# Kernel tuning notes

Measured on AMD Instinct MI355X. Metric: run time of the kernel, lower is better.

## Reference

```python
import jax, jax.numpy as jnp
import numpy as np
from jax import lax

EPS = 1e-5
DN = ('NCHW', 'OIHW', 'NCHW')


def setup_inputs() -> dict:
    key = jax.random.key(0)
    ks = jax.random.split(key, 16)
    B = 8192
    # uniform(0,1): every pixel nonzero => all voxels active => sparse conv == dense conv
    x = jax.random.uniform(ks[0], (B, 1, 28, 28), dtype=jnp.float32)

    def conv_params(kw, kb, c_in, c_out, k):
        scale = 1.0 / np.sqrt(c_in * k * k)
        w = jax.random.normal(kw, (c_out, c_in, k, k), dtype=jnp.float32) * scale
        b = jax.random.normal(kb, (c_out,), dtype=jnp.float32) * scale
        return w, b

    w0, b0 = conv_params(ks[1], ks[2], 1, 32, 3)
    w1, b1 = conv_params(ks[3], ks[4], 32, 64, 2)
    w2, b2 = conv_params(ks[5], ks[6], 64, 128, 2)
    # BatchNorm affine params (init: gamma=1, beta=0)
    g0, be0 = jnp.ones((32,), jnp.float32), jnp.zeros((32,), jnp.float32)
    g1, be1 = jnp.ones((64,), jnp.float32), jnp.zeros((64,), jnp.float32)
    g2, be2 = jnp.ones((128,), jnp.float32), jnp.zeros((128,), jnp.float32)
    w_fc = jax.random.normal(ks[7], (10, 128), dtype=jnp.float32) * (1.0 / np.sqrt(128))
    b_fc = jax.random.normal(ks[8], (10,), dtype=jnp.float32) * (1.0 / np.sqrt(128))
    return dict(x=x, w0=w0, b0=b0, g0=g0, be0=be0,
                w1=w1, b1=b1, g1=g1, be1=be1,
                w2=w2, b2=b2, g2=g2, be2=be2,
                w_fc=w_fc, b_fc=b_fc)


def _conv_bn_relu(x, w, b, g, be, stride, padding):
    # sparse conv on fully-active grid == dense conv
    y = lax.conv_general_dilated(x, w, (stride, stride), padding,
                                 dimension_numbers=DN)
    y = y + b[None, :, None, None]
    # BatchNorm1d over (N_active, C) == stats over batch+spatial (biased var)
    mean = jnp.mean(y, axis=(0, 2, 3))
    var = jnp.var(y, axis=(0, 2, 3))
    y = (y - mean[None, :, None, None]) * lax.rsqrt(var + EPS)[None, :, None, None]
    y = y * g[None, :, None, None] + be[None, :, None, None]
    return jax.nn.relu(y)


def reference(x, w0, b0, g0, be0, w1, b1, g1, be1, w2, b2, g2, be2, w_fc, b_fc):
    h = _conv_bn_relu(x, w0, b0, g0, be0, 1, 'SAME')    # (B,32,28,28)
    h = _conv_bn_relu(h, w1, b1, g1, be1, 2, 'VALID')   # (B,64,14,14)
    h = _conv_bn_relu(h, w2, b2, g2, be2, 2, 'VALID')   # (B,128,7,7)
    pooled = jnp.mean(h, axis=(2, 3))                    # AdaptiveAvgPool2d(1)+Flatten
    return pooled @ w_fc.T + b_fc                        # (B, n_classes)
```

## Files before the change

kernel.cpp:

```cpp
#include <hip/hip_runtime.h>
#include <hip/hip_bf16.h>

typedef __bf16 bf16x8 __attribute__((ext_vector_type(8)));
typedef float  f32x4  __attribute__((ext_vector_type(4)));
typedef float  f32x2  __attribute__((ext_vector_type(2)));

#define BSZ 8192

__device__ __constant__ int d_base2[9] = {0, 5, 9, 13, 16, 19, 21, 23, 24};

__global__ __launch_bounds__(256) void k_stats0(const float* __restrict__ x,
                                                float* __restrict__ part0,
                                                const float* __restrict__ w1,
                                                const float* __restrict__ w2,
                                                __bf16* __restrict__ w1b,
                                                __bf16* __restrict__ w2b) {
    __shared__ float sred[4 * 59];
    const int tid = threadIdx.x;
    {
        int t = blockIdx.x * 256 + tid;
        if (t < 8192) {
            int oc = t >> 7, k = t & 127, c = k & 31, d = k >> 5;
            w1b[t] = (__bf16)w1[oc * 128 + c * 4 + d];
        }
        if (t < 32768) {
            int oc = t >> 8, k = t & 255, c = k & 63, d = k >> 6;
            w2b[t] = (__bf16)w2[oc * 256 + c * 4 + d];
        }
    }
    const int base2[9] = {0, 5, 9, 13, 16, 19, 21, 23, 24};
    const int rsz[9]   = {5, 4, 4, 3, 3, 2, 2, 1, 1};
    f32x2 a2[25];
    float ax[9];
#pragma unroll
    for (int i = 0; i < 25; i++) a2[i] = (f32x2){0.f, 0.f};
#pragma unroll
    for (int i = 0; i < 9; i++) ax[i] = 0.f;
    const int total = BSZ * 784;
    for (int p = blockIdx.x * 256 + tid; p < total; p += gridDim.x * 256) {
        int b = p / 784, pix = p - b * 784;
        int y = pix / 28, xx = pix - y * 28;
        const float* xb = x + (long)b * 784;
        float nv[9];
#pragma unroll
        for (int dy = 0; dy < 3; dy++) {
            int yy = y + dy - 1;
#pragma unroll
            for (int dx = 0; dx < 3; dx++) {
                int x2 = xx + dx - 1;
                nv[dy * 3 + dx] = (yy >= 0 && yy < 28 && x2 >= 0 && x2 < 28) ? xb[yy * 28 + x2] : 0.f;
            }
        }
#pragma unroll
        for (int t = 0; t < 9; t++) {
            float vt = nv[t];
            ax[t] += vt;
            f32x2 vv = {vt, vt};
#pragma unroll
            for (int pp2 = 0; pp2 < 5; pp2++) {
                if (pp2 < rsz[t]) {
                    int u = t + 2 * pp2;
                    f32x2 nn = {nv[u], (u + 1 < 9) ? nv[u + 1] : 0.f};
                    a2[base2[t] + pp2] = __builtin_elementwise_fma(vv, nn, a2[base2[t] + pp2]);
                }
            }
        }
    }
    float outv[59];
#pragma unroll
    for (int i = 0; i < 50; i++) outv[i] = a2[i >> 1][i & 1];
#pragma unroll
    for (int i = 0; i < 9; i++) outv[50 + i] = ax[i];
#pragma unroll
    for (int i = 0; i < 59; i++) {
        float v = outv[i];
        v += __shfl_xor(v, 1);  v += __shfl_xor(v, 2);  v += __shfl_xor(v, 4);
        v += __shfl_xor(v, 8);  v += __shfl_xor(v, 16); v += __shfl_xor(v, 32);
        outv[i] = v;
    }
    const int l = tid & 63, w = tid >> 6;
    if (l == 0) {
#pragma unroll
        for (int i = 0; i < 59; i++) sred[w * 59 + i] = outv[i];
    }
    __syncthreads();
    if (tid < 59)
        part0[blockIdx.x * 64 + tid] = sred[tid] + sred[59 + tid] + sred[118 + tid] + sred[177 + tid];
}

__global__ void k_fin0(const float* __restrict__ part0, const float* __restrict__ w0,
                       const float* __restrict__ g0, const float* __restrict__ be0,
                       float* __restrict__ abc0) {
    __shared__ float red[4 * 59];
    int t = threadIdx.x, c = t & 63, g = t >> 6;
    if (c < 59) {
        float acc = 0.f;
        for (int i = g; i < 1024; i += 4) acc += part0[i * 64 + c];
        red[g * 59 + c] = acc;
    }
    __syncthreads();
    if (t < 59) red[t] = red[t] + red[59 + t] + red[118 + t] + red[177 + t];
    __syncthreads();
    if (t < 32) {
        const int base2[9] = {0, 5, 9, 13, 16, 19, 21, 23, 24};
        float wv[9];
#pragma unroll
        for (int tap = 0; tap < 9; tap++) wv[tap] = w0[t * 9 + tap];
        float sum = 0.f, sq = 0.f;
#pragma unroll
        for (int ta = 0; ta < 9; ta++) {
            sum = fmaf(wv[ta], red[50 + ta], sum);
#pragma unroll
            for (int u = ta; u < 9; u++) {
                float coef = (u == ta) ? 1.f : 2.f;
                float Mv = red[2 * base2[ta] + (u - ta)];
                sq = fmaf(coef * wv[ta] * wv[u], Mv, sq);
            }
        }
        float cnt = (float)BSZ * 784.f;
        float mean = sum / cnt;
        float var = sq / cnt - mean * mean;
        float A = g0[t] * rsqrtf(var + 1e-5f);
#pragma unroll
        for (int tap = 0; tap < 9; tap++)
            abc0[(t >> 3) * 72 + tap * 8 + (t & 7)] = A * wv[tap];
        abc0[288 + t] = be0[t] - mean * A;
    }
}

__global__ __launch_bounds__(256) void k_conv01(const float* __restrict__ x,
                                                const float* __restrict__ abc0,
                                                const __bf16* __restrict__ w1b,
                                                __bf16* __restrict__ h1,
                                                float* __restrict__ part1) {
    __shared__ float xs[30 * 30];
    __shared__ __attribute__((aligned(16))) __bf16 sAt[2][16 * 136];
    const int tid = threadIdx.x;
    if (tid < 116) {
        int idx;
        if (tid < 30)      idx = tid;
        else if (tid < 60) idx = 29 * 30 + (tid - 30);
        else if (tid < 88) idx = (tid - 60 + 1) * 30;
        else               idx = (tid - 88 + 1) * 30 + 29;
        xs[idx] = 0.f;
    }
    const int pgu = __builtin_amdgcn_readfirstlane(tid >> 6);
    const f32x2* wfp = (const f32x2*)(abc0 + pgu * 72);
    f32x2 wf2[36];
#pragma unroll
    for (int i = 0; i < 36; i++) wf2[i] = wfp[i];
    const f32x2* c2p = (const f32x2*)(abc0 + 288 + pgu * 8);
    f32x2 c2[4];
#pragma unroll
    for (int j = 0; j < 4; j++) c2[j] = c2p[j];

    const int pi = tid & 15, pd = (tid >> 4) & 3;
    const int w = tid >> 6, l = tid & 63, q = l >> 4, n = l & 15;
    const int oc = w * 16 + n;
    bf16x8 fbv[4];
#pragma unroll
    for (int kc = 0; kc < 4; kc++)
        fbv[kc] = *(const bf16x8*)&w1b[oc * 128 + kc * 32 + q * 8];
    const f32x2 zero2 = {0.f, 0.f};

    for (int img = 0; img < 4; img++) {
        const int b = blockIdx.x * 4 + img;
        const f32x4* xb4 = (const f32x4*)(x + (long)b * 784);
        if (tid < 196) {
            int yy = tid / 7, xx4 = (tid - yy * 7) * 4;
            f32x4 v4 = xb4[tid];
            float* dst = &xs[(yy + 1) * 30 + xx4 + 1];
            dst[0] = v4[0]; dst[1] = v4[1]; dst[2] = v4[2]; dst[3] = v4[3];
        }
        __syncthreads();
        f32x2 st_s = zero2, st_q = zero2;
        __bf16* hb = h1 + (long)b * 12544 + (q * 4) * 64 + oc;
        for (int mt = 0; mt < 13; mt++) {
            __bf16* dst = &sAt[mt & 1][pi * 136 + pd * 32 + pgu * 8];
            int m = mt * 16 + pi;
            bf16x8 pk;
            if (m < 196) {
                int my = m / 14, mx = m - my * 14;
                int y0 = my * 2 + (pd >> 1), x0 = mx * 2 + (pd & 1);
                float nv[9];
#pragma unroll
                for (int dy = 0; dy < 3; dy++)
#pragma unroll
                    for (int dx = 0; dx < 3; dx++)
                        nv[dy * 3 + dx] = xs[(y0 + dy) * 30 + x0 + dx];
                f32x2 a2[4];
#pragma unroll
                for (int j = 0; j < 4; j++) a2[j] = c2[j];
#pragma unroll
                for (int t = 0; t < 9; t++) {
                    f32x2 vv = {nv[t], nv[t]};
#pragma unroll
                    for (int j = 0; j < 4; j++)
                        a2[j] = __builtin_elementwise_fma(vv, wf2[t * 4 + j], a2[j]);
                }
#pragma unroll
                for (int j = 0; j < 4; j++) {
                    f32x2 mv = __builtin_elementwise_max(a2[j], zero2);
                    pk[2 * j]     = (__bf16)mv[0];
                    pk[2 * j + 1] = (__bf16)mv[1];
                }
            } else {
#pragma unroll
                for (int j = 0; j < 8; j++) pk[j] = (__bf16)0.0f;
            }
            *(bf16x8*)dst = pk;
            __syncthreads();
            const __bf16* sa = &sAt[mt & 1][n * 136 + q * 8];
            f32x4 acc = {0.f, 0.f, 0.f, 0.f};
#pragma unroll
            for (int kc = 0; kc < 4; kc++) {
                bf16x8 fav = *(const bf16x8*)&sa[kc * 32];
                acc = __builtin_amdgcn_mfma_f32_16x16x32_bf16(fav, fbv[kc], acc, 0, 0, 0);
            }
            bool valid = (mt < 12) | (q == 0);
            __bf16* hp = hb + mt * 16 * 64;
            float fv[4];
#pragma unroll
            for (int r = 0; r < 4; r++) {
                __bf16 hv = (__bf16)acc[r];
                if (valid) hp[r * 64] = hv;
                fv[r] = (float)hv;
            }
            f32x2 f01 = {fv[0], fv[1]}, f23 = {fv[2], fv[3]};
            st_s = st_s + f01; st_s = st_s + f23;
            st_q = __builtin_elementwise_fma(f01, f01, st_q);
            st_q = __builtin_elementwise_fma(f23, f23, st_q);
        }
        float ssum = st_s[0] + st_s[1], ssq = st_q[0] + st_q[1];
        ssum += __shfl_xor(ssum, 16); ssum += __shfl_xor(ssum, 32);
        ssq  += __shfl_xor(ssq, 16);  ssq  += __shfl_xor(ssq, 32);
        if (l < 16) {
            part1[(long)oc * BSZ + b] = ssum;
            part1[(long)(64 + oc) * BSZ + b] = ssq;
        }
    }
}

__global__ __launch_bounds__(256) void k_redfin(const float* __restrict__ part,
                                                const float* __restrict__ g,
                                                const float* __restrict__ be,
                                                float* __restrict__ abc,
                                                int C, float cnt) {
    __shared__ float s1[256], s2[256];
    const int c = blockIdx.x, tid = threadIdx.x;
    float a = 0.f, bq = 0.f;
    const float* p1 = part + (long)c * BSZ;
    const float* p2 = part + (long)(C + c) * BSZ;
    for (int i = tid; i < BSZ; i += 256) { a += p1[i]; bq += p2[i]; }
    s1[tid] = a; s2[tid] = bq;
    __syncthreads();
    for (int s = 128; s > 0; s >>= 1) {
        if (tid < s) { s1[tid] += s1[tid + s]; s2[tid] += s2[tid + s]; }
        __syncthreads();
    }
    if (tid == 0) {
        float mean = s1[0] / cnt;
        float var = s2[0] / cnt - mean * mean;
        float A = g[c] * rsqrtf(var + 1e-5f);
        abc[c] = A;
        abc[C + c] = be[c] - mean * A;
    }
}

__global__ __launch_bounds__(256) void k_conv2s(__bf16* __restrict__ h1,
                                                const __bf16* __restrict__ w2b,
                                                const float* __restrict__ abc1,
                                                float* __restrict__ part2) {
    __shared__ __attribute__((aligned(16))) __bf16 sAt[2][16 * 264];
    __shared__ __attribute__((aligned(16))) __bf16 zt[2][16 * 136];
    __shared__ float sbn1[128];
    const int tid = threadIdx.x;
    if (tid < 128) sbn1[tid] = abc1[tid];
    const int w = tid >> 6, l = tid & 63, q = l >> 4, n = l & 15;
    bf16x8 fbv[2][8];
#pragma unroll
    for (int ntl = 0; ntl < 2; ntl++) {
        int oc = (2 * w + ntl) * 16 + n;
#pragma unroll
        for (int kc = 0; kc < 8; kc++)
            fbv[ntl][kc] = *(const bf16x8*)&w2b[oc * 256 + kc * 32 + q * 8];
    }
    __syncthreads();
    const int cpb = (tid & 7) * 8;
    f32x2 A1p[4], C1p[4];
#pragma unroll
    for (int p = 0; p < 4; p++) {
        A1p[p] = (f32x2){sbn1[cpb + 2 * p], sbn1[cpb + 2 * p + 1]};
        C1p[p] = (f32x2){sbn1[64 + cpb + 2 * p], sbn1[64 + cpb + 2 * p + 1]};
    }
    const f32x2 zero2 = {0.f, 0.f};
    const int srow = tid >> 4, so = (tid & 15) * 8;

    for (int img = 0; img < 4; img++) {
        const int b = blockIdx.x * 4 + img;
        __bf16* src = h1 + (long)b * 12544;
        f32x2 st_s[2] = {zero2, zero2}, st_q[2] = {zero2, zero2};
        for (int mt = 0; mt < 4; mt++) {
            if (mt >= 2) {
                int m = (mt - 2) * 16 + srow;
                if (m < 49) {
                    bf16x8 zv = *(const bf16x8*)&zt[mt & 1][srow * 136 + so];
                    *(bf16x8*)&src[m * 128 + so] = zv;
                }
            }
#pragma unroll
            for (int it = 0; it < 2; it++) {
                int idx = it * 256 + tid;
                int rl = idx >> 5, o = (idx & 31) * 8;
                int r = mt * 16 + rl;
                bf16x8 wv;
                if (r < 49) {
                    int d = o >> 6;
                    int c = o & 63;
                    int py = r / 7, px = r - py * 7;
                    int msrc = (2 * py + (d >> 1)) * 14 + 2 * px + (d & 1);
                    bf16x8 v = *(const bf16x8*)&src[msrc * 64 + c];
#pragma unroll
                    for (int p = 0; p < 4; p++) {
                        f32x2 vf = {(float)v[2 * p], (float)v[2 * p + 1]};
                        f32x2 rr = __builtin_elementwise_fma(vf, A1p[p], C1p[p]);
                        rr = __builtin_elementwise_max(rr, zero2);
                        wv[2 * p]     = (__bf16)rr[0];
                        wv[2 * p + 1] = (__bf16)rr[1];
                    }
                } else {
#pragma unroll
                    for (int j = 0; j < 8; j++) wv[j] = (__bf16)0.0f;
                }
                *(bf16x8*)&sAt[mt & 1][rl * 264 + o] = wv;
            }
            __syncthreads();
            bf16x8 fav[8];
#pragma unroll
            for (int kc = 0; kc < 8; kc++)
                fav[kc] = *(const bf16x8*)&sAt[mt & 1][n * 264 + kc * 32 + q * 8];
#pragma unroll
            for (int ntl = 0; ntl < 2; ntl++) {
                f32x4 acc = {0.f, 0.f, 0.f, 0.f};
#pragma unroll
                for (int kc = 0; kc < 8; kc++)
                    acc = __builtin_amdgcn_mfma_f32_16x16x32_bf16(fav[kc], fbv[ntl][kc], acc, 0, 0, 0);
                float fv[4];
#pragma unroll
                for (int rr = 0; rr < 4; rr++) {
                    __bf16 hv = (__bf16)acc[rr];
                    zt[mt & 1][(q * 4 + rr) * 136 + (2 * w + ntl) * 16 + n] = hv;
                    fv[rr] = (float)hv;
                }
                f32x2 f01 = {fv[0], fv[1]}, f23 = {fv[2], fv[3]};
                st_s[ntl] = st_s[ntl] + f01; st_s[ntl] = st_s[ntl] + f23;
                st_q[ntl] = __builtin_elementwise_fma(f01, f01, st_q[ntl]);
                st_q[ntl] = __builtin_elementwise_fma(f23, f23, st_q[ntl]);
            }
        }
        __syncthreads();
        {
            int m2 = 32 + srow;
            if (m2 < 49) {
                bf16x8 zv = *(const bf16x8*)&zt[0][srow * 136 + so];
                *(bf16x8*)&src[m2 * 128 + so] = zv;
            }
            int m3 = 48 + srow;
            if (m3 < 49) {
                bf16x8 zv = *(const bf16x8*)&zt[1][srow * 136 + so];
                *(bf16x8*)&src[m3 * 128 + so] = zv;
            }
        }
#pragma unroll
        for (int ntl = 0; ntl < 2; ntl++) {
            float ssum = st_s[ntl][0] + st_s[ntl][1];
            float ssq  = st_q[ntl][0] + st_q[ntl][1];
            ssum += __shfl_xor(ssum, 16); ssum += __shfl_xor(ssum, 32);
            ssq  += __shfl_xor(ssq, 16);  ssq  += __shfl_xor(ssq, 32);
            if (l < 16) {
                int oc = (2 * w + ntl) * 16 + l;
                part2[(long)oc * BSZ + b] = ssum;
                part2[(long)(128 + oc) * BSZ + b] = ssq;
            }
        }
    }
}

__global__ __launch_bounds__(256) void k_final(const __bf16* __restrict__ z2,
                                               const float* __restrict__ abc2,
                                               const float* __restrict__ wfc,
                                               const float* __restrict__ bfc,
                                               float* __restrict__ out) {
    __shared__ float sbn2[256];
    __shared__ float pp[16 * 128];
    __shared__ float pooled[128];
    __shared__ float fcred[80];
    const int tid = threadIdx.x;
    sbn2[tid] = abc2[tid];
    __syncthreads();
    const int g = tid & 15, c0 = g * 8, rg = tid >> 4;
    f32x2 A2p[4], C2p[4];
#pragma unroll
    for (int p = 0; p < 4; p++) {
        A2p[p] = (f32x2){sbn2[c0 + 2 * p], sbn2[c0 + 2 * p + 1]};
        C2p[p] = (f32x2){sbn2[128 + c0 + 2 * p], sbn2[128 + c0 + 2 * p + 1]};
    }
    const f32x2 zero2 = {0.f, 0.f};
    for (int img = 0; img < 4; img++) {
        const int b = blockIdx.x * 4 + img;
        const __bf16* src = z2 + (long)b * 12544;
        f32x2 acc2[4];
#pragma unroll
        for (int p = 0; p < 4; p++) acc2[p] = zero2;
        for (int rr = rg; rr < 49; rr += 16) {
            bf16x8 v = *(const bf16x8*)&src[rr * 128 + c0];
#pragma unroll
            for (int p = 0; p < 4; p++) {
                f32x2 vf = {(float)v[2 * p], (float)v[2 * p + 1]};
                f32x2 t0 = __builtin_elementwise_fma(vf, A2p[p], C2p[p]);
                t0 = __builtin_elementwise_max(t0, zero2);
                acc2[p] = acc2[p] + t0;
            }
        }
        f32x4 lo = {acc2[0][0], acc2[0][1], acc2[1][0], acc2[1][1]};
        f32x4 hi = {acc2[2][0], acc2[2][1], acc2[3][0], acc2[3][1]};
        *(f32x4*)&pp[rg * 128 + c0]     = lo;
        *(f32x4*)&pp[rg * 128 + c0 + 4] = hi;
        __syncthreads();
        if (tid < 128) {
            float s = 0.f;
#pragma unroll
            for (int r = 0; r < 16; r++) s += pp[r * 128 + tid];
            pooled[tid] = s * (1.f / 49.f);
        }
        __syncthreads();
        if (tid < 80) {
            int o = tid >> 3, s = tid & 7;
            float a = 0.f;
#pragma unroll
            for (int j = 0; j < 16; j++) a = fmaf(pooled[s * 16 + j], wfc[o * 128 + s * 16 + j], a);
            fcred[tid] = a;
        }
        __syncthreads();
        if (tid < 10) {
            float a = bfc[tid];
#pragma unroll
            for (int s = 0; s < 8; s++) a += fcred[tid * 8 + s];
            out[(long)b * 10 + tid] = a;
        }
    }
}

extern "C" void kernel_launch(void* const* d_in, const int* in_sizes, int n_in,
                              void* d_out, int out_size, void* d_ws, size_t ws_size,
                              hipStream_t stream) {
    const float* x   = (const float*)d_in[0];
    const float* w0  = (const float*)d_in[1];
    const float* g0  = (const float*)d_in[3];
    const float* be0 = (const float*)d_in[4];
    const float* w1  = (const float*)d_in[5];
    const float* g1  = (const float*)d_in[7];
    const float* be1 = (const float*)d_in[8];
    const float* w2  = (const float*)d_in[9];
    const float* g2  = (const float*)d_in[11];
    const float* be2 = (const float*)d_in[12];
    const float* wfc = (const float*)d_in[13];
    const float* bfc = (const float*)d_in[14];
    float* out = (float*)d_out;

    float* ws    = (float*)d_ws;
    float* part0 = ws;
    float* abc0  = part0 + 1024 * 64;
    float* part1 = abc0 + 320;
    float* abc1  = part1 + 128 * BSZ;
    float* part2 = abc1 + 128;
    float* abc2  = part2 + 256 * BSZ;
    __bf16* w1b  = (__bf16*)(abc2 + 256);
    __bf16* w2b  = w1b + 8192;
    __bf16* h1   = w2b + 32768;

    k_stats0<<<dim3(1024), dim3(256), 0, stream>>>(x, part0, w1, w2, w1b, w2b);
    k_fin0<<<dim3(1), dim3(256), 0, stream>>>(part0, w0, g0, be0, abc0);
    k_conv01<<<dim3(BSZ / 4), dim3(256), 0, stream>>>(x, abc0, w1b, h1, part1);
    k_redfin<<<dim3(64), dim3(256), 0, stream>>>(part1, g1, be1, abc1, 64, (float)(BSZ * 196));
    k_conv2s<<<dim3(BSZ / 4), dim3(256), 0, stream>>>(h1, w2b, abc1, part2);
    k_redfin<<<dim3(128), dim3(256), 0, stream>>>(part2, g2, be2, abc2, 128, (float)(BSZ * 49));
    k_final<<<dim3(BSZ / 4), dim3(256), 0, stream>>>(h1, abc2, wfc, bfc, out);
}
```

Measured before the change: 410.3 us.

## Fold BN statistic finalization into producer kernels via atomics and last-block pattern

Measured after the change: 895.0 us. 2.18x slower.

```diff
diff --git a/kernel.cpp b/kernel.cpp
--- a/kernel.cpp
+++ b/kernel.cpp
@@ -7,18 +7,22 @@
 
 #define BSZ 8192
 
-__device__ __constant__ int d_base2[9] = {0, 5, 9, 13, 16, 19, 21, 23, 24};
 
 __global__ __launch_bounds__(256) void k_stats0(const float* __restrict__ x,
-                                                float* __restrict__ part0,
+                                                float* __restrict__ ctrl,
+                                                const float* __restrict__ w0,
+                                                const float* __restrict__ g0,
+                                                const float* __restrict__ be0,
+                                                float* __restrict__ abc0,
                                                 const float* __restrict__ w1,
                                                 const float* __restrict__ w2,
                                                 __bf16* __restrict__ w1b,
                                                 __bf16* __restrict__ w2b) {
     __shared__ float sred[4 * 59];
-    const int tid = threadIdx.x;
+    __shared__ int slast;
+    const int tid = threadIdx.x, blk = blockIdx.x;
     {
-        int t = blockIdx.x * 256 + tid;
+        int t = blk * 256 + tid;
         if (t < 8192) {
             int oc = t >> 7, k = t & 127, c = k & 31, d = k >> 5;
             w1b[t] = (__bf16)w1[oc * 128 + c * 4 + d];
@@ -37,7 +41,7 @@
 #pragma unroll
     for (int i = 0; i < 9; i++) ax[i] = 0.f;
     const int total = BSZ * 784;
-    for (int p = blockIdx.x * 256 + tid; p < total; p += gridDim.x * 256) {
+    for (int p = blk * 256 + tid; p < total; p += gridDim.x * 256) {
         int b = p / 784, pix = p - b * 784;
         int y = pix / 28, xx = pix - y * 28;
         const float* xb = x + (long)b * 784;
@@ -52,16 +56,16 @@
             }
         }
 #pragma unroll
-        for (int t = 0; t < 9; t++) {
-            float vt = nv[t];
-            ax[t] += vt;
+        for (int t2 = 0; t2 < 9; t2++) {
+            float vt = nv[t2];
+            ax[t2] += vt;
             f32x2 vv = {vt, vt};
 #pragma unroll
             for (int pp2 = 0; pp2 < 5; pp2++) {
-                if (pp2 < rsz[t]) {
-                    int u = t + 2 * pp2;
+                if (pp2 < rsz[t2]) {
+                    int u = t2 + 2 * pp2;
                     f32x2 nn = {nv[u], (u + 1 < 9) ? nv[u + 1] : 0.f};
-                    a2[base2[t] + pp2] = __builtin_elementwise_fma(vv, nn, a2[base2[t] + pp2]);
+                    a2[base2[t2] + pp2] = __builtin_elementwise_fma(vv, nn, a2[base2[t2] + pp2]);
                 }
             }
         }
@@ -85,46 +89,42 @@
     }
     __syncthreads();
     if (tid < 59)
-        part0[blockIdx.x * 64 + tid] = sred[tid] + sred[59 + tid] + sred[118 + tid] + sred[177 + tid];
-}
-
-__global__ void k_fin0(const float* __restrict__ part0, const float* __restrict__ w0,
-                       const float* __restrict__ g0, const float* __restrict__ be0,
-                       float* __restrict__ abc0) {
-    __shared__ float red[4 * 59];
-    int t = threadIdx.x, c = t & 63, g = t >> 6;
-    if (c < 59) {
-        float acc = 0.f;
-        for (int i = g; i < 1024; i += 4) acc += part0[i * 64 + c];
-        red[g * 59 + c] = acc;
+        atomicAdd(&ctrl[tid], sred[tid] + sred[59 + tid] + sred[118 + tid] + sred[177 + tid]);
+    __threadfence();
+    if (tid == 0) {
+        int old = atomicAdd((int*)&ctrl[448], 1);
+        slast = (old == (int)gridDim.x - 1) ? 1 : 0;
     }
     __syncthreads();
-    if (t < 59) red[t] = red[t] + red[59 + t] + red[118 + t] + red[177 + t];
-    __syncthreads();
-    if (t < 32) {
-        const int base2[9] = {0, 5, 9, 13, 16, 19, 21, 23, 24};
-        float wv[9];
-#pragma unroll
-        for (int tap = 0; tap < 9; tap++) wv[tap] = w0[t * 9 + tap];
-        float sum = 0.f, sq = 0.f;
-#pragma unroll
-        for (int ta = 0; ta < 9; ta++) {
-            sum = fmaf(wv[ta], red[50 + ta], sum);
-#pragma unroll
-            for (int u = ta; u < 9; u++) {
-                float coef = (u == ta) ? 1.f : 2.f;
-                float Mv = red[2 * base2[ta] + (u - ta)];
-                sq = fmaf(coef * wv[ta] * wv[u], Mv, sq);
-            }
-        }
-        float cnt = (float)BSZ * 784.f;
-        float mean = sum / cnt;
-        float var = sq / cnt - mean * mean;
-        float A = g0[t] * rsqrtf(var + 1e-5f);
-#pragma unroll
-        for (int tap = 0; tap < 9; tap++)
-            abc0[(t >> 3) * 72 + tap * 8 + (t & 7)] = A * wv[tap];
-        abc0[288 + t] = be0[t] - mean * A;
+    if (slast) {
+        __threadfence();
+        __shared__ float red[59];
+        if (tid < 59) red[tid] = atomicAdd(&ctrl[tid], 0.f);
+        __syncthreads();
+        if (tid < 32) {
+            float wv[9];
+#pragma unroll
+            for (int tap = 0; tap < 9; tap++) wv[tap] = w0[tid * 9 + tap];
+            float sum = 0.f, sq = 0.f;
+#pragma unroll
+            for (int ta = 0; ta < 9; ta++) {
+                sum = fmaf(wv[ta], red[50 + ta], sum);
+#pragma unroll
+                for (int u = ta; u < 9; u++) {
+                    float coef = (u == ta) ? 1.f : 2.f;
+                    float Mv = red[2 * base2[ta] + (u - ta)];
+                    sq = fmaf(coef * wv[ta] * wv[u], Mv, sq);
+                }
+            }
+            float cnt = (float)BSZ * 784.f;
+            float mean = sum / cnt;
+            float var = sq / cnt - mean * mean;
+            float A = g0[tid] * rsqrtf(var + 1e-5f);
+#pragma unroll
+            for (int tap = 0; tap < 9; tap++)
+                abc0[(tid >> 3) * 72 + tap * 8 + (tid & 7)] = A * wv[tap];
+            abc0[288 + tid] = be0[tid] - mean * A;
+        }
     }
 }
 
@@ -132,9 +132,13 @@
                                                 const float* __restrict__ abc0,
                                                 const __bf16* __restrict__ w1b,
                                                 __bf16* __restrict__ h1,
-                                                float* __restrict__ part1) {
+                                                float* __restrict__ ctrl,
+                                                const float* __restrict__ g1,
+                                                const float* __restrict__ be1,
+                                                float* __restrict__ abc1) {
     __shared__ float xs[30 * 30];
     __shared__ __attribute__((aligned(16))) __bf16 sAt[2][16 * 136];
+    __shared__ int slast;
     const int tid = threadIdx.x;
     if (tid < 116) {
         int idx;
@@ -162,6 +166,7 @@
     for (int kc = 0; kc < 4; kc++)
         fbv[kc] = *(const bf16x8*)&w1b[oc * 128 + kc * 32 + q * 8];
     const f32x2 zero2 = {0.f, 0.f};
+    f32x2 st_s = zero2, st_q = zero2;
 
     for (int img = 0; img < 4; img++) {
         const int b = blockIdx.x * 4 + img;
@@ -173,7 +178,6 @@
             dst[0] = v4[0]; dst[1] = v4[1]; dst[2] = v4[2]; dst[3] = v4[3];
         }
         __syncthreads();
-        f32x2 st_s = zero2, st_q = zero2;
         __bf16* hb = h1 + (long)b * 12544 + (q * 4) * 64 + oc;
         for (int mt = 0; mt < 13; mt++) {
             __bf16* dst = &sAt[mt & 1][pi * 136 + pd * 32 + pgu * 8];
@@ -231,49 +235,47 @@
             st_q = __builtin_elementwise_fma(f01, f01, st_q);
             st_q = __builtin_elementwise_fma(f23, f23, st_q);
         }
-        float ssum = st_s[0] + st_s[1], ssq = st_q[0] + st_q[1];
-        ssum += __shfl_xor(ssum, 16); ssum += __shfl_xor(ssum, 32);
-        ssq  += __shfl_xor(ssq, 16);  ssq  += __shfl_xor(ssq, 32);
-        if (l < 16) {
-            part1[(long)oc * BSZ + b] = ssum;
-            part1[(long)(64 + oc) * BSZ + b] = ssq;
-        }
-    }
-}
-
-__global__ __launch_bounds__(256) void k_redfin(const float* __restrict__ part,
-                                                const float* __restrict__ g,
-                                                const float* __restrict__ be,
-                                                float* __restrict__ abc,
-                                                int C, float cnt) {
-    __shared__ float s1[256], s2[256];
-    const int c = blockIdx.x, tid = threadIdx.x;
-    float a = 0.f, bq = 0.f;
-    const float* p1 = part + (long)c * BSZ;
-    const float* p2 = part + (long)(C + c) * BSZ;
-    for (int i = tid; i < BSZ; i += 256) { a += p1[i]; bq += p2[i]; }
-    s1[tid] = a; s2[tid] = bq;
+        __syncthreads();
+    }
+    float ssum = st_s[0] + st_s[1], ssq = st_q[0] + st_q[1];
+    ssum += __shfl_xor(ssum, 16); ssum += __shfl_xor(ssum, 32);
+    ssq  += __shfl_xor(ssq, 16);  ssq  += __shfl_xor(ssq, 32);
+    if (l < 16) {
+        atomicAdd(&ctrl[64 + oc], ssum);
+        atomicAdd(&ctrl[64 + 64 + oc], ssq);
+    }
+    __threadfence();
+    if (tid == 0) {
+        int old = atomicAdd((int*)&ctrl[449], 1);
+        slast = (old == (int)gridDim.x - 1) ? 1 : 0;
+    }
     __syncthreads();
-    for (int s = 128; s > 0; s >>= 1) {
-        if (tid < s) { s1[tid] += s1[tid + s]; s2[tid] += s2[tid + s]; }
-        __syncthreads();
-    }
-    if (tid == 0) {
-        float mean = s1[0] / cnt;
-        float var = s2[0] / cnt - mean * mean;
-        float A = g[c] * rsqrtf(var + 1e-5f);
-        abc[c] = A;
-        abc[C + c] = be[c] - mean * A;
+    if (slast) {
+        __threadfence();
+        if (tid < 64) {
+            float sum = atomicAdd(&ctrl[64 + tid], 0.f);
+            float sq  = atomicAdd(&ctrl[128 + tid], 0.f);
+            float cnt = (float)(BSZ * 196);
+            float mean = sum / cnt;
+            float var = sq / cnt - mean * mean;
+            float A = g1[tid] * rsqrtf(var + 1e-5f);
+            abc1[tid] = A;
+            abc1[64 + tid] = be1[tid] - mean * A;
+        }
     }
 }
 
 __global__ __launch_bounds__(256) void k_conv2s(__bf16* __restrict__ h1,
                                                 const __bf16* __restrict__ w2b,
                                                 const float* __restrict__ abc1,
-                                                float* __restrict__ part2) {
+                                                float* __restrict__ ctrl,
+                                                const float* __restrict__ g2,
+                                                const float* __restrict__ be2,
+                                                float* __restrict__ abc2) {
     __shared__ __attribute__((aligned(16))) __bf16 sAt[2][16 * 264];
     __shared__ __attribute__((aligned(16))) __bf16 zt[2][16 * 136];
     __shared__ float sbn1[128];
+    __shared__ int slast;
     const int tid = threadIdx.x;
     if (tid < 128) sbn1[tid] = abc1[tid];
     const int w = tid >> 6, l = tid & 63, q = l >> 4, n = l & 15;
@@ -295,11 +297,11 @@
     }
     const f32x2 zero2 = {0.f, 0.f};
     const int srow = tid >> 4, so = (tid & 15) * 8;
+    f32x2 st_s[2] = {zero2, zero2}, st_q[2] = {zero2, zero2};
 
     for (int img = 0; img < 4; img++) {
         const int b = blockIdx.x * 4 + img;
         __bf16* src = h1 + (long)b * 12544;
-        f32x2 st_s[2] = {zero2, zero2}, st_q[2] = {zero2, zero2};
         for (int mt = 0; mt < 4; mt++) {
             if (mt >= 2) {
                 int m = (mt - 2) * 16 + srow;
@@ -371,17 +373,36 @@
                 *(bf16x8*)&src[m3 * 128 + so] = zv;
             }
         }
-#pragma unroll
-        for (int ntl = 0; ntl < 2; ntl++) {
-            float ssum = st_s[ntl][0] + st_s[ntl][1];
-            float ssq  = st_q[ntl][0] + st_q[ntl][1];
-            ssum += __shfl_xor(ssum, 16); ssum += __shfl_xor(ssum, 32);
-            ssq  += __shfl_xor(ssq, 16);  ssq  += __shfl_xor(ssq, 32);
-            if (l < 16) {
-                int oc = (2 * w + ntl) * 16 + l;
-                part2[(long)oc * BSZ + b] = ssum;
-                part2[(long)(128 + oc) * BSZ + b] = ssq;
-            }
+    }
+#pragma unroll
+    for (int ntl = 0; ntl < 2; ntl++) {
+        float ssum = st_s[ntl][0] + st_s[ntl][1];
+        float ssq  = st_q[ntl][0] + st_q[ntl][1];
+        ssum += __shfl_xor(ssum, 16); ssum += __shfl_xor(ssum, 32);
+        ssq  += __shfl_xor(ssq, 16);  ssq  += __shfl_xor(ssq, 32);
+        if (l < 16) {
+            int oc = (2 * w + ntl) * 16 + l;
+            atomicAdd(&ctrl[192 + oc], ssum);
+            atomicAdd(&ctrl[192 + 128 + oc], ssq);
+        }
+    }
+    __threadfence();
+    if (tid == 0) {
+        int old = atomicAdd((int*)&ctrl[450], 1);
+        slast = (old == (int)gridDim.x - 1) ? 1 : 0;
+    }
+    __syncthreads();
+    if (slast) {
+        __threadfence();
+        if (tid < 128) {
+            float sum = atomicAdd(&ctrl[192 + tid], 0.f);
+            float sq  = atomicAdd(&ctrl[320 + tid], 0.f);
+            float cnt = (float)(BSZ * 49);
+            float mean = sum / cnt;
+            float var = sq / cnt - mean * mean;
+            float A = g2[tid] * rsqrtf(var + 1e-5f);
+            abc2[tid] = A;
+            abc2[128 + tid] = be2[tid] - mean * A;
         }
     }
 }
@@ -448,6 +469,7 @@
             for (int s = 0; s < 8; s++) a += fcred[tid * 8 + s];
             out[(long)b * 10 + tid] = a;
         }
+        __syncthreads();
     }
 }
 
@@ -468,22 +490,17 @@
     const float* bfc = (const float*)d_in[14];
     float* out = (float*)d_out;
 
-    float* ws    = (float*)d_ws;
-    float* part0 = ws;
-    float* abc0  = part0 + 1024 * 64;
-    float* part1 = abc0 + 320;
-    float* abc1  = part1 + 128 * BSZ;
-    float* part2 = abc1 + 128;
-    float* abc2  = part2 + 256 * BSZ;
+    float* ctrl  = (float*)d_ws;
+    float* abc0  = ctrl + 512;
+    float* abc1  = abc0 + 320;
+    float* abc2  = abc1 + 128;
     __bf16* w1b  = (__bf16*)(abc2 + 256);
     __bf16* w2b  = w1b + 8192;
     __bf16* h1   = w2b + 32768;
 
-    k_stats0<<<dim3(1024), dim3(256), 0, stream>>>(x, part0, w1, w2, w1b, w2b);
-    k_fin0<<<dim3(1), dim3(256), 0, stream>>>(part0, w0, g0, be0, abc0);
-    k_conv01<<<dim3(BSZ / 4), dim3(256), 0, stream>>>(x, abc0, w1b, h1, part1);
-    k_redfin<<<dim3(64), dim3(256), 0, stream>>>(part1, g1, be1, abc1, 64, (float)(BSZ * 196));
-    k_conv2s<<<dim3(BSZ / 4), dim3(256), 0, stream>>>(h1, w2b, abc1, part2);
-    k_redfin<<<dim3(128), dim3(256), 0, stream>>>(part2, g2, be2, abc2, 128, (float)(BSZ * 49));
+    hipMemsetAsync(ctrl, 0, 2048, stream);
+    k_stats0<<<dim3(1024), dim3(256), 0, stream>>>(x, ctrl, w0, g0, be0, abc0, w1, w2, w1b, w2b);
+    k_conv01<<<dim3(BSZ / 4), dim3(256), 0, stream>>>(x, abc0, w1b, h1, ctrl, g1, be1, abc1);
+    k_conv2s<<<dim3(BSZ / 4), dim3(256), 0, stream>>>(h1, w2b, abc1, ctrl, g2, be2, abc2);
     k_final<<<dim3(BSZ / 4), dim3(256), 0, stream>>>(h1, abc2, wfc, bfc, out);
 }
```
